# Kernel tuning notes

Measured on AMD Instinct MI355X. Metric: run time of the kernel, lower is better.

Reference implementation:

```python
import jax, jax.numpy as jnp
import numpy as np

B, N, M, D = 64, 512, 1024, 128

def setup_inputs() -> dict:
    key = jax.random.key(0)
    ks = jax.random.split(key, 7)
    s = 1.0 / np.sqrt(D)
    return {
        "h_c": jax.random.normal(ks[0], (B, N, D), dtype=jnp.float32),
        "h_p": jax.random.normal(ks[1], (B, M, D), dtype=jnp.float32),
        "U_w": jax.random.normal(ks[2], (D, D), dtype=jnp.float32) * s,
        "U_b": jax.random.normal(ks[3], (D,), dtype=jnp.float32) * s,
        "V_w": jax.random.normal(ks[4], (D, D), dtype=jnp.float32) * s,
        "V_b": jax.random.normal(ks[5], (D,), dtype=jnp.float32) * s,
        "q": jax.random.normal(ks[6], (D,), dtype=jnp.float32),
    }

def reference(h_c, h_p, U_w, U_b, V_w, V_b, q):
    # ReLU-activated linear projections (torch Linear: x @ W.T + b)
    Uc = jax.nn.relu(jnp.einsum('bnd,ed->bne', h_c, U_w) + U_b)  # (B,N,D)
    Vp = jax.nn.relu(jnp.einsum('bmd,ed->bme', h_p, V_w) + V_b)  # (B,M,D)
    # bilinear attention scores and softmax over protein axis
    attn = jnp.einsum('bnd,bmd->bnm', Uc, Vp)                    # (B,N,M)
    weights = jax.nn.softmax(attn, axis=-1)
    context = jnp.einsum('bnm,bmd->bnd', weights, Vp)            # (B,N,D)
    joint = (Uc + context) * q                                   # (B,N,D)
    return joint.mean(axis=1)                                    # (B,D)
```

## Files before the change

### kernel.cpp

```cpp
#include <hip/hip_runtime.h>
#include <hip/hip_bf16.h>
#include <cstdint>

#define BB 64
#define NN 512
#define MM 1024
#define DD 128

typedef __bf16 bf16x8 __attribute__((ext_vector_type(8)));
typedef float f32x4 __attribute__((ext_vector_type(4)));

static __device__ __forceinline__ unsigned short f2bf(float f) {
    union { float f; unsigned int i; } v; v.f = f;
    unsigned int x = v.i;
    x += 0x7FFFu + ((x >> 16) & 1u);
    return (unsigned short)(x >> 16);
}
static __device__ __forceinline__ unsigned int f2bf2(float a, float b) {
    union { __hip_bfloat162 h; unsigned int u; } c;
    c.h = __float22bfloat162_rn(make_float2(a, b));
    return c.u;
}
static __device__ __forceinline__ void async16(const void* g, void* l) {
    __builtin_amdgcn_global_load_lds(
        (const __attribute__((address_space(1))) void*)g,
        (__attribute__((address_space(3))) void*)l, 16, 0, 0);
}

__global__ __launch_bounds__(256) void wcvt_kernel(
    const float* __restrict__ Wu, const float* __restrict__ Wv,
    unsigned short* __restrict__ out)
{
    const float* W = blockIdx.x ? Wv : Wu;
    unsigned short* o = out + blockIdx.x * 16384;
    const float s = blockIdx.x ? 1.0f : 1.44269504088896f;
    #pragma unroll
    for (int i = 0; i < 8; ++i) {
        int ch = i * 256 + threadIdx.x;
        int r = ch >> 4, c = ch & 15;
        const float4* src = (const float4*)(W + r * 128 + c * 8);
        float4 a = src[0], b = src[1];
        uint4 v = { f2bf2(a.x * s, a.y * s), f2bf2(a.z * s, a.w * s),
                    f2bf2(b.x * s, b.y * s), f2bf2(b.z * s, b.w * s) };
        *(uint4*)&o[r * 128 + ((c ^ (r & 7)) << 3)] = v;
    }
}

__global__ __launch_bounds__(256, 4) void proj_v_kernel(
    const float* __restrict__ X,
    const unsigned short* __restrict__ Wvb,
    const float* __restrict__ bias,
    unsigned short* __restrict__ Y,
    unsigned short* __restrict__ YT)
{
    __shared__ __align__(16) unsigned short Ws[17408];
    unsigned short* Ys = Ws;
    unsigned short* Ts = Ws + 8192;
    const int t = threadIdx.x;
    const int lane = t & 63;
    const int wave = t >> 6;
    const int n16 = lane & 15, q = lane >> 4;
    const long row0 = (long)blockIdx.x * 64;

    float4 xv[8];
    {
        const float* xrow = X + (row0 + wave * 16 + n16) * DD + q * 8;
        #pragma unroll
        for (int kk = 0; kk < 4; ++kk) {
            xv[2 * kk]     = *(const float4*)(xrow + kk * 32);
            xv[2 * kk + 1] = *(const float4*)(xrow + kk * 32 + 4);
        }
    }
    #pragma unroll
    for (int i = 0; i < 8; ++i)
        async16(Wvb + (wave * 512 + i * 64 + lane) * 8, Ws + wave * 4096 + i * 512);
    __syncthreads();

    f32x4 acc[8];
    #pragma unroll
    for (int j = 0; j < 8; ++j) acc[j] = {0.f, 0.f, 0.f, 0.f};

    #pragma unroll
    for (int kk = 0; kk < 4; ++kk) {
        float4 x0 = xv[2 * kk], x1 = xv[2 * kk + 1];
        union { bf16x8 v; unsigned int u[4]; } a;
        a.u[0] = f2bf2(x0.x, x0.y); a.u[1] = f2bf2(x0.z, x0.w);
        a.u[2] = f2bf2(x1.x, x1.y); a.u[3] = f2bf2(x1.z, x1.w);
        #pragma unroll
        for (int j = 0; j < 8; ++j) {
            bf16x8 b = *(const bf16x8*)&Ws[(j * 16 + n16) * 128
                                           + (((q + 4 * kk) ^ (n16 & 7)) << 3)];
            acc[j] = __builtin_amdgcn_mfma_f32_16x16x32_bf16(a.v, b, acc[j], 0, 0, 0);
        }
    }

    unsigned short yb[8][4];
    #pragma unroll
    for (int j = 0; j < 8; ++j) {
        const float bv = bias[j * 16 + n16];
        float y[4];
        #pragma unroll
        for (int r = 0; r < 4; ++r) {
            float v = acc[j][r] + bv;
            y[r] = v > 0.f ? v : 0.f;
        }
        uint2 u = { f2bf2(y[0], y[1]), f2bf2(y[2], y[3]) };
        *(uint2*)&yb[j][0] = u;
    }
    __syncthreads();

    #pragma unroll
    for (int j = 0; j < 8; ++j) {
        const int e = j * 16 + n16;
        #pragma unroll
        for (int r = 0; r < 4; ++r)
            Ys[(wave * 16 + q * 4 + r) * 128 + e] = yb[j][r];
        *(uint2*)&Ts[e * 72 + wave * 16 + q * 4] = *(uint2*)&yb[j][0];
    }
    __syncthreads();

    {
        uint4* dstY = (uint4*)(Y + row0 * DD);
        const long b = row0 >> 10;
        const long mt = (row0 & 1023) >> 6;
        uint4* dstT = (uint4*)(YT + ((b * 16 + mt) * 128) * 64);
        #pragma unroll
        for (int i = 0; i < 4; ++i) {
            int idx = i * 256 + t;
            dstY[idx] = ((const uint4*)Ys)[idx];
            int e = idx >> 3, m = (idx & 7) * 8;
            dstT[idx] = *(const uint4*)&Ts[e * 72 + m];
        }
    }
}

static __device__ __forceinline__ void bar_lgkm() {
    asm volatile("s_waitcnt lgkmcnt(0)" ::: "memory");
    __builtin_amdgcn_s_barrier();
    __builtin_amdgcn_sched_barrier(0);
}

static __device__ __forceinline__ void attn_iter(
    int mt, unsigned short* smem, unsigned short* Ps,
    const unsigned short* __restrict__ vpb,
    const unsigned short* __restrict__ vtb,
    int wave, int lane, int n16, int q, int a_off,
    const bf16x8 (&Bg)[4][4],
    bf16x8 (&aC)[4], bf16x8 (&aN)[4],
    f32x4 (&O)[8], float (&lpart)[4])
{
    const int nx = (mt + 1 > 15) ? 15 : mt + 1;
    {
        const unsigned short* st = vtb + nx * 8192;
        unsigned short* dst = smem + ((mt + 1) & 1) * 8192 + wave * 2048;
        #pragma unroll
        for (int i = 0; i < 4; ++i) {
            int L = wave * 256 + i * 64 + lane;
            int r = L >> 3, sc = L & 7, c = sc ^ (r & 7);
            async16(st + r * 64 + c * 8, dst + i * 512);
        }
    }
    __builtin_amdgcn_sched_barrier(0);
    {
        const unsigned short* pa = vpb + nx * 8192 + a_off;
        #pragma unroll
        for (int kk = 0; kk < 4; ++kk)
            aN[kk] = *(const bf16x8*)(pa + kk * 32);
    }

    f32x4 S[4];
    #pragma unroll
    for (int j = 0; j < 4; ++j) S[j] = {0.f, 0.f, 0.f, 0.f};
    __builtin_amdgcn_s_setprio(1);
    #pragma unroll
    for (int kk = 0; kk < 4; ++kk) {
        #pragma unroll
        for (int j = 0; j < 4; ++j)
            S[j] = __builtin_amdgcn_mfma_f32_16x16x32_bf16(aC[kk], Bg[j][kk], S[j], 0, 0, 0);
    }
    __builtin_amdgcn_s_setprio(0);

    #pragma unroll
    for (int j = 0; j < 4; ++j) {
        float p0 = __builtin_exp2f(S[j][0]);
        float p1 = __builtin_exp2f(S[j][1]);
        float p2 = __builtin_exp2f(S[j][2]);
        float p3 = __builtin_exp2f(S[j][3]);
        lpart[j] += (p0 + p1) + (p2 + p3);
        uint2 u = { f2bf2(p0, p1), f2bf2(p2, p3) };
        *(uint2*)&Ps[(j * 16 + n16) * 72 + wave * 16 + q * 4] = u;
    }
    bar_lgkm();

    const unsigned short* VTs = smem + (mt & 1) * 8192;
    __builtin_amdgcn_s_setprio(1);
    #pragma unroll
    for (int kk = 0; kk < 2; ++kk) {
        bf16x8 a = *(const bf16x8*)&Ps[(wave * 16 + n16) * 72 + kk * 32 + q * 8];
        #pragma unroll
        for (int j = 0; j < 8; ++j) {
            bf16x8 bb = *(const bf16x8*)&VTs[(j * 16 + n16) * 64 + ((kk * 4 + q) ^ (n16 & 7)) * 8];
            O[j] = __builtin_amdgcn_mfma_f32_16x16x32_bf16(a, bb, O[j], 0, 0, 0);
        }
    }
    __builtin_amdgcn_s_setprio(0);
    asm volatile("s_waitcnt vmcnt(4) lgkmcnt(0)" ::: "memory");
    __builtin_amdgcn_s_barrier();
    __builtin_amdgcn_sched_barrier(0);
}

__global__ __launch_bounds__(256, 2) void attn_kernel(
    const float* __restrict__ hc,
    const unsigned short* __restrict__ Wub,
    const float* __restrict__ Ub,
    const unsigned short* __restrict__ Vp,
    const unsigned short* __restrict__ VpT,
    float* __restrict__ part)
{
    __shared__ __align__(16) unsigned short smem[24576];
    unsigned short* Ws  = smem;
    unsigned short* Ucs = smem + 16384;
    unsigned short* Ps  = smem + 16384;

    const int t = threadIdx.x;
    const int lane = t & 63;
    const int wave = t >> 6;
    const int n16 = lane & 15, q = lane >> 4;

    const int id = blockIdx.x;
    const int xcd = id & 7;
    const int slot = id >> 3;
    const int b = xcd * 8 + (slot >> 3);
    const int nt = slot & 7;

    const unsigned short* vpb = Vp + (long)b * MM * DD;
    const unsigned short* vtb = VpT + (long)b * MM * DD;

    const float LOG2E = 1.44269504088896f;
    const float RLN2  = 0.69314718055994531f;

    float4 xv[8];
    {
        const float* xrow = hc + ((long)b * NN + nt * 64 + wave * 16 + n16) * DD + q * 8;
        #pragma unroll
        for (int kk = 0; kk < 4; ++kk) {
            xv[2 * kk]     = *(const float4*)(xrow + kk * 32);
            xv[2 * kk + 1] = *(const float4*)(xrow + kk * 32 + 4);
        }
    }
    #pragma unroll
    for (int i = 0; i < 8; ++i)
        async16(Wub + (wave * 512 + i * 64 + lane) * 8, Ws + wave * 4096 + i * 512);
    __syncthreads();

    f32x4 acc[8];
    #pragma unroll
    for (int j = 0; j < 8; ++j) acc[j] = {0.f, 0.f, 0.f, 0.f};
    #pragma unroll
    for (int kk = 0; kk < 4; ++kk) {
        float4 x0 = xv[2 * kk], x1 = xv[2 * kk + 1];
        union { bf16x8 v; unsigned int u[4]; } a;
        a.u[0] = f2bf2(x0.x, x0.y); a.u[1] = f2bf2(x0.z, x0.w);
        a.u[2] = f2bf2(x1.x, x1.y); a.u[3] = f2bf2(x1.z, x1.w);
        #pragma unroll
        for (int j = 0; j < 8; ++j) {
            bf16x8 bb = *(const bf16x8*)&Ws[(j * 16 + n16) * 128
                                            + (((q + 4 * kk) ^ (n16 & 7)) << 3)];
            acc[j] = __builtin_amdgcn_mfma_f32_16x16x32_bf16(a.v, bb, acc[j], 0, 0, 0);
        }
    }
    float ucred[8];
    #pragma unroll
    for (int j = 0; j < 8; ++j) {
        const float bv = Ub[j * 16 + n16] * LOG2E;
        float s = 0.f;
        #pragma unroll
        for (int r = 0; r < 4; ++r) {
            float v = acc[j][r] + bv;
            v = v > 0.f ? v : 0.f;
            s += v;
            int row = wave * 16 + q * 4 + r;
            int pc = (2 * j + (n16 >> 3)) ^ (row & 7);
            Ucs[row * 128 + pc * 8 + (n16 & 7)] = f2bf(v);
        }
        ucred[j] = s;
    }
    __syncthreads();

    bf16x8 Bg[4][4];
    #pragma unroll
    for (int j = 0; j < 4; ++j)
        #pragma unroll
        for (int kk = 0; kk < 4; ++kk)
            Bg[j][kk] = *(const bf16x8*)&Ucs[(j * 16 + n16) * 128
                                             + (((q + 4 * kk) ^ (n16 & 7)) << 3)];

    const int a_off = (wave * 16 + n16) * 128 + q * 8;
    bf16x8 aA[4], aB[4];
    #pragma unroll
    for (int kk = 0; kk < 4; ++kk)
        aA[kk] = *(const bf16x8*)&vpb[a_off + kk * 32];
    {
        unsigned short* dst = smem + wave * 2048;
        #pragma unroll
        for (int i = 0; i < 4; ++i) {
            int L = wave * 256 + i * 64 + lane;
            int r = L >> 3, sc = L & 7, c = sc ^ (r & 7);
            async16(vtb + r * 64 + c * 8, dst + i * 512);
        }
    }
    asm volatile("s_waitcnt vmcnt(0) lgkmcnt(0)" ::: "memory");
    __builtin_amdgcn_s_barrier();
    __builtin_amdgcn_sched_barrier(0);

    f32x4 O[8];
    #pragma unroll
    for (int j = 0; j < 8; ++j) O[j] = {0.f, 0.f, 0.f, 0.f};
    float lpart[4] = {0.f, 0.f, 0.f, 0.f};

    #pragma unroll 1
    for (int mt = 0; mt < 16; mt += 2) {
        attn_iter(mt,     smem, Ps, vpb, vtb, wave, lane, n16, q, a_off, Bg, aA, aB, O, lpart);
        attn_iter(mt + 1, smem, Ps, vpb, vtb, wave, lane, n16, q, a_off, Bg, aB, aA, O, lpart);
    }

    #pragma unroll
    for (int j = 0; j < 4; ++j) {
        lpart[j] += __shfl_xor(lpart[j], 16);
        lpart[j] += __shfl_xor(lpart[j], 32);
    }
    float* lred = (float*)Ps;
    float* red  = (float*)Ps + 256;
    if (q == 0) {
        #pragma unroll
        for (int j = 0; j < 4; ++j)
            lred[wave * 64 + j * 16 + n16] = lpart[j];
    }
    __syncthreads();

    float inv[4];
    #pragma unroll
    for (int r = 0; r < 4; ++r) {
        int n = wave * 16 + q * 4 + r;
        inv[r] = 1.0f / (lred[n] + lred[64 + n] + lred[128 + n] + lred[192 + n]);
    }

    #pragma unroll
    for (int j = 0; j < 8; ++j) {
        float s = ucred[j] * RLN2
                + O[j][0] * inv[0] + O[j][1] * inv[1]
                + O[j][2] * inv[2] + O[j][3] * inv[3];
        s += __shfl_xor(s, 16);
        s += __shfl_xor(s, 32);
        if (q == 0)
            red[wave * 128 + j * 16 + n16] = s;
    }
    __syncthreads();
    if (t < 128) {
        float tot = red[t] + red[128 + t] + red[256 + t] + red[384 + t];
        part[(long)(b * 8 + nt) * DD + t] = tot;
    }
}

__global__ __launch_bounds__(256) void finalize_kernel(
    const float* __restrict__ part, const float* __restrict__ qv,
    float* __restrict__ out)
{
    int i = blockIdx.x * 256 + threadIdx.x;
    int b = i >> 7, d = i & 127;
    const float* p = part + (long)b * 8 * DD + d;
    float s = 0.f;
    #pragma unroll
    for (int nt = 0; nt < 8; ++nt) s += p[nt * DD];
    out[i] = s * qv[d] * (1.0f / (float)NN);
}

extern "C" void kernel_launch(void* const* d_in, const int* in_sizes, int n_in,
                              void* d_out, int out_size, void* d_ws, size_t ws_size,
                              hipStream_t stream) {
    const float* h_c = (const float*)d_in[0];
    const float* h_p = (const float*)d_in[1];
    const float* U_w = (const float*)d_in[2];
    const float* U_b = (const float*)d_in[3];
    const float* V_w = (const float*)d_in[4];
    const float* V_b = (const float*)d_in[5];
    const float* qv  = (const float*)d_in[6];
    float* out = (float*)d_out;

    unsigned short* Vp  = (unsigned short*)d_ws;
    unsigned short* VpT = Vp + (size_t)BB * MM * DD;
    float* part = (float*)(VpT + (size_t)BB * MM * DD);
    unsigned short* Wcv = (unsigned short*)(part + (size_t)BB * 8 * DD);

    wcvt_kernel<<<2, 256, 0, stream>>>(U_w, V_w, Wcv);
    proj_v_kernel<<<BB * MM / 64, 256, 0, stream>>>(h_p, Wcv + 16384, V_b, Vp, VpT);
    attn_kernel<<<512, 256, 0, stream>>>(h_c, Wcv, U_b, Vp, VpT, part);
    finalize_kernel<<<32, 256, 0, stream>>>(part, qv, out);
}
```

Baseline: 136.1 us.

## Move Uc projection into proj kernel and triple-buffer attention loop

The h_c projection (Uc = relu(h_c U^T + b)) moves out of the attention kernel into the shared projection kernel, which gains extra blocks that write bf16 Uc to global memory plus per-tile column sums. The finalize kernel adds those column sums back in. The attention loop switches to three rotating V^T LDS buffers and two P buffers, which removes one barrier per iteration and relaxes the vmcnt wait. This shortens the attention kernel's prologue and its synchronisation, at the cost of an extra global round trip for Uc and more LDS per block.

```diff
diff --git a/kernel.cpp b/kernel.cpp
--- a/kernel.cpp
+++ b/kernel.cpp
@@ -46,12 +46,16 @@
     }
 }
 
-__global__ __launch_bounds__(256, 4) void proj_v_kernel(
-    const float* __restrict__ X,
-    const unsigned short* __restrict__ Wvb,
-    const float* __restrict__ bias,
+__global__ __launch_bounds__(256, 4) void proj_kernel(
+    const float* __restrict__ hp,
+    const float* __restrict__ hc,
+    const unsigned short* __restrict__ Wcv,
+    const float* __restrict__ Ub,
+    const float* __restrict__ Vb,
     unsigned short* __restrict__ Y,
-    unsigned short* __restrict__ YT)
+    unsigned short* __restrict__ YT,
+    unsigned short* __restrict__ Ucg,
+    float* __restrict__ colsum)
 {
     __shared__ __align__(16) unsigned short Ws[17408];
     unsigned short* Ys = Ws;
@@ -60,7 +64,14 @@
     const int lane = t & 63;
     const int wave = t >> 6;
     const int n16 = lane & 15, q = lane >> 4;
-    const long row0 = (long)blockIdx.x * 64;
+    const bool isC = blockIdx.x >= (BB * MM / 64);
+    const float LOG2E = 1.44269504088896f;
+
+    const long row0 = isC ? (long)(blockIdx.x - BB * MM / 64) * 64
+                          : (long)blockIdx.x * 64;
+    const float* X = isC ? hc : hp;
+    const unsigned short* Wb = isC ? Wcv : (Wcv + 16384);
+    const float* bias = isC ? Ub : Vb;
 
     float4 xv[8];
     {
@@ -73,7 +84,7 @@
     }
     #pragma unroll
     for (int i = 0; i < 8; ++i)
-        async16(Wvb + (wave * 512 + i * 64 + lane) * 8, Ws + wave * 4096 + i * 512);
+        async16(Wb + (wave * 512 + i * 64 + lane) * 8, Ws + wave * 4096 + i * 512);
     __syncthreads();
 
     f32x4 acc[8];
@@ -95,31 +106,34 @@
     }
 
     unsigned short yb[8][4];
+    float colp[8];
     #pragma unroll
     for (int j = 0; j < 8; ++j) {
-        const float bv = bias[j * 16 + n16];
-        float y[4];
+        const float bv = isC ? bias[j * 16 + n16] * LOG2E : bias[j * 16 + n16];
+        float y[4], s = 0.f;
         #pragma unroll
         for (int r = 0; r < 4; ++r) {
             float v = acc[j][r] + bv;
-            y[r] = v > 0.f ? v : 0.f;
-        }
+            v = v > 0.f ? v : 0.f;
+            y[r] = v;
+            s += v;
+        }
+        colp[j] = s;
         uint2 u = { f2bf2(y[0], y[1]), f2bf2(y[2], y[3]) };
         *(uint2*)&yb[j][0] = u;
     }
     __syncthreads();
 
-    #pragma unroll
-    for (int j = 0; j < 8; ++j) {
-        const int e = j * 16 + n16;
-        #pragma unroll
-        for (int r = 0; r < 4; ++r)
-            Ys[(wave * 16 + q * 4 + r) * 128 + e] = yb[j][r];
-        *(uint2*)&Ts[e * 72 + wave * 16 + q * 4] = *(uint2*)&yb[j][0];
-    }
-    __syncthreads();
-
-    {
+    if (!isC) {
+        #pragma unroll
+        for (int j = 0; j < 8; ++j) {
+            const int e = j * 16 + n16;
+            #pragma unroll
+            for (int r = 0; r < 4; ++r)
+                Ys[(wave * 16 + q * 4 + r) * 128 + e] = yb[j][r];
+            *(uint2*)&Ts[e * 72 + wave * 16 + q * 4] = *(uint2*)&yb[j][0];
+        }
+        __syncthreads();
         uint4* dstY = (uint4*)(Y + row0 * DD);
         const long b = row0 >> 10;
         const long mt = (row0 & 1023) >> 6;
@@ -131,17 +145,40 @@
             int e = idx >> 3, m = (idx & 7) * 8;
             dstT[idx] = *(const uint4*)&Ts[e * 72 + m];
         }
-    }
-}
-
-static __device__ __forceinline__ void bar_lgkm() {
-    asm volatile("s_waitcnt lgkmcnt(0)" ::: "memory");
-    __builtin_amdgcn_s_barrier();
-    __builtin_amdgcn_sched_barrier(0);
+    } else {
+        #pragma unroll
+        for (int j = 0; j < 8; ++j) {
+            colp[j] += __shfl_xor(colp[j], 16);
+            colp[j] += __shfl_xor(colp[j], 32);
+        }
+        float* cs = (float*)Ts;
+        if (q == 0) {
+            #pragma unroll
+            for (int j = 0; j < 8; ++j)
+                cs[wave * 128 + j * 16 + n16] = colp[j];
+        }
+        #pragma unroll
+        for (int j = 0; j < 8; ++j) {
+            const int e = j * 16 + n16;
+            #pragma unroll
+            for (int r = 0; r < 4; ++r)
+                Ys[(wave * 16 + q * 4 + r) * 128 + e] = yb[j][r];
+        }
+        __syncthreads();
+        const int c = (int)(row0 >> 6);
+        uint4* dstU = (uint4*)(Ucg + row0 * DD);
+        #pragma unroll
+        for (int i = 0; i < 4; ++i) {
+            int idx = i * 256 + t;
+            dstU[idx] = ((const uint4*)Ys)[idx];
+        }
+        if (t < 128)
+            colsum[(long)c * DD + t] = cs[t] + cs[128 + t] + cs[256 + t] + cs[384 + t];
+    }
 }
 
 static __device__ __forceinline__ void attn_iter(
-    int mt, unsigned short* smem, unsigned short* Ps,
+    int mt, unsigned short* bD, const unsigned short* bR, unsigned short* Ps,
     const unsigned short* __restrict__ vpb,
     const unsigned short* __restrict__ vtb,
     int wave, int lane, int n16, int q, int a_off,
@@ -152,7 +189,7 @@
     const int nx = (mt + 1 > 15) ? 15 : mt + 1;
     {
         const unsigned short* st = vtb + nx * 8192;
-        unsigned short* dst = smem + ((mt + 1) & 1) * 8192 + wave * 2048;
+        unsigned short* dst = bD + wave * 2048;
         #pragma unroll
         for (int i = 0; i < 4; ++i) {
             int L = wave * 256 + i * 64 + lane;
@@ -190,37 +227,32 @@
         uint2 u = { f2bf2(p0, p1), f2bf2(p2, p3) };
         *(uint2*)&Ps[(j * 16 + n16) * 72 + wave * 16 + q * 4] = u;
     }
-    bar_lgkm();
-
-    const unsigned short* VTs = smem + (mt & 1) * 8192;
+    asm volatile("s_waitcnt vmcnt(8) lgkmcnt(0)" ::: "memory");
+    __builtin_amdgcn_s_barrier();
+    __builtin_amdgcn_sched_barrier(0);
+
     __builtin_amdgcn_s_setprio(1);
     #pragma unroll
     for (int kk = 0; kk < 2; ++kk) {
         bf16x8 a = *(const bf16x8*)&Ps[(wave * 16 + n16) * 72 + kk * 32 + q * 8];
         #pragma unroll
         for (int j = 0; j < 8; ++j) {
-            bf16x8 bb = *(const bf16x8*)&VTs[(j * 16 + n16) * 64 + ((kk * 4 + q) ^ (n16 & 7)) * 8];
+            bf16x8 bb = *(const bf16x8*)&bR[(j * 16 + n16) * 64 + ((kk * 4 + q) ^ (n16 & 7)) * 8];
             O[j] = __builtin_amdgcn_mfma_f32_16x16x32_bf16(a, bb, O[j], 0, 0, 0);
         }
     }
     __builtin_amdgcn_s_setprio(0);
-    asm volatile("s_waitcnt vmcnt(4) lgkmcnt(0)" ::: "memory");
-    __builtin_amdgcn_s_barrier();
-    __builtin_amdgcn_sched_barrier(0);
 }
 
 __global__ __launch_bounds__(256, 2) void attn_kernel(
-    const float* __restrict__ hc,
-    const unsigned short* __restrict__ Wub,
-    const float* __restrict__ Ub,
+    const unsigned short* __restrict__ Ucg,
     const unsigned short* __restrict__ Vp,
     const unsigned short* __restrict__ VpT,
     float* __restrict__ part)
 {
-    __shared__ __align__(16) unsigned short smem[24576];
-    unsigned short* Ws  = smem;
-    unsigned short* Ucs = smem + 16384;
-    unsigned short* Ps  = smem + 16384;
+    __shared__ __align__(16) unsigned short smem[33792];
+    unsigned short* Ps0 = smem + 24576;
+    unsigned short* Ps1 = smem + 29184;
 
     const int t = threadIdx.x;
     const int lane = t & 63;
@@ -235,65 +267,14 @@
 
     const unsigned short* vpb = Vp + (long)b * MM * DD;
     const unsigned short* vtb = VpT + (long)b * MM * DD;
-
-    const float LOG2E = 1.44269504088896f;
-    const float RLN2  = 0.69314718055994531f;
-
-    float4 xv[8];
-    {
-        const float* xrow = hc + ((long)b * NN + nt * 64 + wave * 16 + n16) * DD + q * 8;
-        #pragma unroll
-        for (int kk = 0; kk < 4; ++kk) {
-            xv[2 * kk]     = *(const float4*)(xrow + kk * 32);
-            xv[2 * kk + 1] = *(const float4*)(xrow + kk * 32 + 4);
-        }
-    }
-    #pragma unroll
-    for (int i = 0; i < 8; ++i)
-        async16(Wub + (wave * 512 + i * 64 + lane) * 8, Ws + wave * 4096 + i * 512);
-    __syncthreads();
-
-    f32x4 acc[8];
-    #pragma unroll
-    for (int j = 0; j < 8; ++j) acc[j] = {0.f, 0.f, 0.f, 0.f};
-    #pragma unroll
-    for (int kk = 0; kk < 4; ++kk) {
-        float4 x0 = xv[2 * kk], x1 = xv[2 * kk + 1];
-        union { bf16x8 v; unsigned int u[4]; } a;
-        a.u[0] = f2bf2(x0.x, x0.y); a.u[1] = f2bf2(x0.z, x0.w);
-        a.u[2] = f2bf2(x1.x, x1.y); a.u[3] = f2bf2(x1.z, x1.w);
-        #pragma unroll
-        for (int j = 0; j < 8; ++j) {
-            bf16x8 bb = *(const bf16x8*)&Ws[(j * 16 + n16) * 128
-                                            + (((q + 4 * kk) ^ (n16 & 7)) << 3)];
-            acc[j] = __builtin_amdgcn_mfma_f32_16x16x32_bf16(a.v, bb, acc[j], 0, 0, 0);
-        }
-    }
-    float ucred[8];
-    #pragma unroll
-    for (int j = 0; j < 8; ++j) {
-        const float bv = Ub[j * 16 + n16] * LOG2E;
-        float s = 0.f;
-        #pragma unroll
-        for (int r = 0; r < 4; ++r) {
-            float v = acc[j][r] + bv;
-            v = v > 0.f ? v : 0.f;
-            s += v;
-            int row = wave * 16 + q * 4 + r;
-            int pc = (2 * j + (n16 >> 3)) ^ (row & 7);
-            Ucs[row * 128 + pc * 8 + (n16 & 7)] = f2bf(v);
-        }
-        ucred[j] = s;
-    }
-    __syncthreads();
+    const unsigned short* ucb = Ucg + ((long)b * NN + nt * 64) * DD;
 
     bf16x8 Bg[4][4];
     #pragma unroll
     for (int j = 0; j < 4; ++j)
         #pragma unroll
         for (int kk = 0; kk < 4; ++kk)
-            Bg[j][kk] = *(const bf16x8*)&Ucs[(j * 16 + n16) * 128
-                                             + (((q + 4 * kk) ^ (n16 & 7)) << 3)];
+            Bg[j][kk] = *(const bf16x8*)&ucb[(j * 16 + n16) * 128 + kk * 32 + q * 8];
 
     const int a_off = (wave * 16 + n16) * 128 + q * 8;
     bf16x8 aA[4], aB[4];
@@ -318,10 +299,15 @@
     for (int j = 0; j < 8; ++j) O[j] = {0.f, 0.f, 0.f, 0.f};
     float lpart[4] = {0.f, 0.f, 0.f, 0.f};
 
+    unsigned short* bR = smem;
+    unsigned short* bD = smem + 8192;
+    unsigned short* bT = smem + 16384;
     #pragma unroll 1
     for (int mt = 0; mt < 16; mt += 2) {
-        attn_iter(mt,     smem, Ps, vpb, vtb, wave, lane, n16, q, a_off, Bg, aA, aB, O, lpart);
-        attn_iter(mt + 1, smem, Ps, vpb, vtb, wave, lane, n16, q, a_off, Bg, aB, aA, O, lpart);
+        attn_iter(mt, bD, bR, Ps0, vpb, vtb, wave, lane, n16, q, a_off, Bg, aA, aB, O, lpart);
+        unsigned short* tp = bR; bR = bD; bD = bT; bT = tp;
+        attn_iter(mt + 1, bD, bR, Ps1, vpb, vtb, wave, lane, n16, q, a_off, Bg, aB, aA, O, lpart);
+        tp = bR; bR = bD; bD = bT; bT = tp;
     }
 
     #pragma unroll
@@ -329,8 +315,8 @@
         lpart[j] += __shfl_xor(lpart[j], 16);
         lpart[j] += __shfl_xor(lpart[j], 32);
     }
-    float* lred = (float*)Ps;
-    float* red  = (float*)Ps + 256;
+    float* lred = (float*)Ps0;
+    float* red  = lred + 256;
     if (q == 0) {
         #pragma unroll
         for (int j = 0; j < 4; ++j)
@@ -347,8 +333,7 @@
 
     #pragma unroll
     for (int j = 0; j < 8; ++j) {
-        float s = ucred[j] * RLN2
-                + O[j][0] * inv[0] + O[j][1] * inv[1]
+        float s = O[j][0] * inv[0] + O[j][1] * inv[1]
                 + O[j][2] * inv[2] + O[j][3] * inv[3];
         s += __shfl_xor(s, 16);
         s += __shfl_xor(s, 32);
@@ -363,16 +348,17 @@
 }
 
 __global__ __launch_bounds__(256) void finalize_kernel(
-    const float* __restrict__ part, const float* __restrict__ qv,
-    float* __restrict__ out)
+    const float* __restrict__ part, const float* __restrict__ colsum,
+    const float* __restrict__ qv, float* __restrict__ out)
 {
     int i = blockIdx.x * 256 + threadIdx.x;
     int b = i >> 7, d = i & 127;
-    const float* p = part + (long)b * 8 * DD + d;
-    float s = 0.f;
-    #pragma unroll
-    for (int nt = 0; nt < 8; ++nt) s += p[nt * DD];
-    out[i] = s * qv[d] * (1.0f / (float)NN);
+    const float* p  = part   + (long)b * 8 * DD + d;
+    const float* cs = colsum + (long)b * 8 * DD + d;
+    float s = 0.f, u = 0.f;
+    #pragma unroll
+    for (int nt = 0; nt < 8; ++nt) { s += p[nt * DD]; u += cs[nt * DD]; }
+    out[i] = (s + u * 0.69314718055994531f) * qv[d] * (1.0f / (float)NN);
 }
 
 extern "C" void kernel_launch(void* const* d_in, const int* in_sizes, int n_in,
@@ -389,11 +375,14 @@
 
     unsigned short* Vp  = (unsigned short*)d_ws;
     unsigned short* VpT = Vp + (size_t)BB * MM * DD;
-    float* part = (float*)(VpT + (size_t)BB * MM * DD);
-    unsigned short* Wcv = (unsigned short*)(part + (size_t)BB * 8 * DD);
+    unsigned short* Ucg = VpT + (size_t)BB * MM * DD;
+    float* part   = (float*)(Ucg + (size_t)BB * NN * DD);
+    float* colsum = part + (size_t)BB * 8 * DD;
+    unsigned short* Wcv = (unsigned short*)(colsum + (size_t)BB * 8 * DD);
 
     wcvt_kernel<<<2, 256, 0, stream>>>(U_w, V_w, Wcv);
-    proj_v_kernel<<<BB * MM / 64, 256, 0, stream>>>(h_p, Wcv + 16384, V_b, Vp, VpT);
-    attn_kernel<<<512, 256, 0, stream>>>(h_c, Wcv, U_b, Vp, VpT, part);
-    finalize_kernel<<<32, 256, 0, stream>>>(part, qv, out);
-}
+    proj_kernel<<<BB * MM / 64 + BB * NN / 64, 256, 0, stream>>>(
+        h_p, h_c, Wcv, U_b, V_b, Vp, VpT, Ucg, colsum);
+    attn_kernel<<<512, 256, 0, stream>>>(Ucg, Vp, VpT, part);
+    finalize_kernel<<<32, 256, 0, stream>>>(part, colsum, qv, out);
+}
```

New measurement: 141.7 us. 4.1% more time.
